# Kernel optimization log

Measured on AMD Instinct MI355X. Metric: run time of the kernel, lower is better.

The kernel has to match this reference:

```python
import jax, jax.numpy as jnp
import numpy as np

B, I, C, K, L = 4, 4, 256, 7, 5
SIZES = [160, 80, 40, 20, 10]


def setup_inputs() -> dict:
    key = jax.random.key(0)
    ks = jax.random.split(key, 10)
    inp = {}
    for i, s in enumerate(SIZES):
        inp[f"feats_x{i}"] = jax.random.normal(ks[i], (B, C, s, s), jnp.float32)
    inp["modulator"] = jax.random.normal(ks[5], (B, I, C, K, K), jnp.float32)
    # conv weights ~ normal_init(std=0.01), biases zero
    inp["pm_w"] = 0.01 * jax.random.normal(ks[6], (L, C, C, K, K), jnp.float32)
    inp["pm_b"] = jnp.zeros((L, C), jnp.float32)
    inp["po_w"] = 0.01 * jax.random.normal(ks[7], (L, C, C), jnp.float32)
    inp["po_b"] = jnp.zeros((L, C), jnp.float32)
    return inp


def reference(feats_x0, feats_x1, feats_x2, feats_x3, feats_x4,
              modulator, pm_w, pm_b, po_w, po_b):
    """Batched version of RPN_Modulator.inference: for every (image i, instance j,
    level k): q = Conv7x7(modulator[i,j]) -> [C,1,1]; out = Conv1x1(q * feats_x[k][i]).
    Vectorized over images and instances instead of nested Python loops."""
    feats = [feats_x0, feats_x1, feats_x2, feats_x3, feats_x4]
    outs = []
    for k in range(L):
        # 7x7 valid conv on a 7x7 crop == full contraction -> per-instance channel vector
        q = jnp.einsum('bichw,ochw->bio', modulator, pm_w[k]) + pm_b[k]  # [B,I,C]
        # channel-wise modulation of the gallery feature map
        m = q[:, :, :, None, None] * feats[k][:, None]                   # [B,I,C,H,W]
        # 1x1 output projection
        o = jnp.einsum('bichw,oc->biohw', m, po_w[k]) \
            + po_b[k][None, None, :, None, None]                          # [B,I,C,H,W]
        outs.append(o)
    return tuple(outs)
```

## Files before the change

### kernel.cpp

```cpp
#include <hip/hip_runtime.h>
#include <hip/hip_bf16.h>


typedef __bf16 bf16x8 __attribute__((ext_vector_type(8)));
typedef float  f32x4  __attribute__((ext_vector_type(4)));
typedef float  f32x16 __attribute__((ext_vector_type(16)));
typedef unsigned short u16;

__device__ __forceinline__ unsigned pack2(float lo, float hi) {
    __hip_bfloat162 h = __float22bfloat162_rn(make_float2(lo, hi));
    union { __hip_bfloat162 h; unsigned u; } cv; cv.h = h; return cv.u;
}

__device__ __forceinline__ void decode_tile(int x, int& k, int& nt, int& N, size_t& oo) {
    if (x < 200)      { k = 0; nt = x;       N = 25600; oo = 0; }
    else if (x < 250) { k = 1; nt = x - 200; N = 6400;  oo = 104857600; }
    else if (x < 263) { k = 2; nt = x - 250; N = 1600;  oo = 131072000; }
    else if (x < 267) { k = 3; nt = x - 263; N = 400;   oo = 137625600; }
    else              { k = 4; nt = x - 267; N = 100;   oo = 139264000; }
}

__global__ __launch_bounds__(256) void k_q(
    const float* __restrict__ modulator,
    const float* __restrict__ pm_w,
    float* __restrict__ qpart)
{
    int o4 = blockIdx.x;
    int k  = blockIdx.y;
    int s  = blockIdx.z;
    int t  = threadIdx.x;
    float acc[4][16];
#pragma unroll
    for (int j = 0; j < 4; ++j)
#pragma unroll
        for (int bi = 0; bi < 16; ++bi) acc[j][bi] = 0.f;
    const float4* mod4 = (const float4*)modulator;
    const float4* wp0 = (const float4*)(pm_w + ((size_t)k * 256 + o4      ) * 12544);
    const float4* wp1 = (const float4*)(pm_w + ((size_t)k * 256 + o4 +  64) * 12544);
    const float4* wp2 = (const float4*)(pm_w + ((size_t)k * 256 + o4 + 128) * 12544);
    const float4* wp3 = (const float4*)(pm_w + ((size_t)k * 256 + o4 + 192) * 12544);
    for (int it = 0; it < 4; ++it) {
        int jj = it * 256 + t;
        if (jj < 784) {
            int jx = s * 784 + jj;
            float4 wv0 = wp0[jx], wv1 = wp1[jx], wv2 = wp2[jx], wv3 = wp3[jx];
#pragma unroll
            for (int bi = 0; bi < 16; ++bi) {
                float4 m = mod4[bi * 3136 + jx];
                acc[0][bi] += wv0.x * m.x + wv0.y * m.y + wv0.z * m.z + wv0.w * m.w;
                acc[1][bi] += wv1.x * m.x + wv1.y * m.y + wv1.z * m.z + wv1.w * m.w;
                acc[2][bi] += wv2.x * m.x + wv2.y * m.y + wv2.z * m.z + wv2.w * m.w;
                acc[3][bi] += wv3.x * m.x + wv3.y * m.y + wv3.z * m.z + wv3.w * m.w;
            }
        }
    }
#pragma unroll
    for (int j = 0; j < 4; ++j)
#pragma unroll
        for (int bi = 0; bi < 16; ++bi)
#pragma unroll
            for (int off = 32; off > 0; off >>= 1)
                acc[j][bi] += __shfl_down(acc[j][bi], off);
    __shared__ float red[4][64];
    int w = t >> 6, lane = t & 63;
    if (lane == 0) {
#pragma unroll
        for (int j = 0; j < 4; ++j)
#pragma unroll
            for (int bi = 0; bi < 16; ++bi) red[w][j * 16 + bi] = acc[j][bi];
    }
    __syncthreads();
    if (t < 64) {
        float v = red[0][t] + red[1][t] + red[2][t] + red[3][t];
        int bi = t & 15;
        int o  = o4 + (t >> 4) * 64;
        qpart[(((size_t)s * 5 + k) * 16 + bi) * 256 + o] = v;
    }
}

__global__ __launch_bounds__(256) void k_w2(
    const float* __restrict__ po_w,
    const float* __restrict__ pm_b,
    const float* __restrict__ qpart,
    u16* __restrict__ w2)
{
    int idx4 = blockIdx.x * 256 + threadIdx.x;
    int c4 = idx4 & 63;
    int o  = (idx4 >> 6) & 255;
    int bi = (idx4 >> 14) & 15;
    int k  = idx4 >> 18;
    size_t qi = ((size_t)(k * 16 + bi)) * 256 + c4 * 4;
    f32x4 q0 = *(const f32x4*)(qpart + qi);
    f32x4 q1 = *(const f32x4*)(qpart + qi + 20480);
    f32x4 q2 = *(const f32x4*)(qpart + qi + 40960);
    f32x4 q3 = *(const f32x4*)(qpart + qi + 61440);
    f32x4 pb = *(const f32x4*)(pm_b + k * 256 + c4 * 4);
    f32x4 q  = q0 + q1 + q2 + q3 + pb;
    f32x4 w  = *(const f32x4*)(po_w + ((size_t)(k * 256 + o)) * 256 + c4 * 4);
    uint2 r;
    r.x = pack2(w[0] * q[0], w[1] * q[1]);
    r.y = pack2(w[2] * q[2], w[3] * q[3]);
    *(uint2*)(w2 + (size_t)idx4 * 4) = r;
}

__global__ __launch_bounds__(512, 4) void k_gemm(
    const float* __restrict__ f0, const float* __restrict__ f1,
    const float* __restrict__ f2, const float* __restrict__ f3,
    const float* __restrict__ f4,
    const u16* __restrict__ w2,
    const float* __restrict__ po_b,
    float* __restrict__ out)
{
    __shared__ __align__(16) u16 ldsB[128 * 256];
    int k, nt, N; size_t oo;
    decode_tile(blockIdx.x, k, nt, N, oo);
    const float* fsrc = (k == 0) ? f0 : (k == 1) ? f1 : (k == 2) ? f2 : (k == 3) ? f3 : f4;
    const int b = blockIdx.y;
    const int t = threadIdx.x;
    const int n0 = nt * 128;

    {
        const int ng = t & 31, grp = t >> 5;
        const bool inb = (n0 + ng * 4) < N;
        const float* s = fsrc + (size_t)b * 256 * N + n0 + ng * 4;
#pragma unroll
        for (int j = 0; j < 4; ++j) {
            int q = j * 16 + grp;
            f32x4 v0 = {0.f,0.f,0.f,0.f}, v1 = {0.f,0.f,0.f,0.f};
            f32x4 v2 = {0.f,0.f,0.f,0.f}, v3 = {0.f,0.f,0.f,0.f};
            if (inb) {
                v0 = *(const f32x4*)(s + (size_t)(4 * q + 0) * N);
                v1 = *(const f32x4*)(s + (size_t)(4 * q + 1) * N);
                v2 = *(const f32x4*)(s + (size_t)(4 * q + 2) * N);
                v3 = *(const f32x4*)(s + (size_t)(4 * q + 3) * N);
            }
#pragma unroll
            for (int e = 0; e < 4; ++e) {
                int n = ng * 4 + e;
                unsigned h = ((unsigned)n & 7u) ^ (((unsigned)n >> 2) & 7u);
                unsigned off = ((unsigned)n << 9) + ((unsigned)q << 3);
                off ^= (h << 4);
                uint2 wv; wv.x = pack2(v0[e], v1[e]); wv.y = pack2(v2[e], v3[e]);
                *(uint2*)((char*)ldsB + off) = wv;
            }
        }
    }
    __syncthreads();

    const int lane = t & 63, w = t >> 6;
    const int l31 = lane & 31, lg5 = lane >> 5;
    const float* pb = po_b + k * 256;
    float* obase0 = out + oo;

    f32x4 bias4[4];
#pragma unroll
    for (int m = 0; m < 4; ++m)
        bias4[m] = *(const f32x4*)(pb + w * 32 + 8 * m + 4 * lg5);

    unsigned mrow[4], mx[4];
#pragma unroll
    for (int ni = 0; ni < 4; ++ni) {
        int row = ni * 32 + l31;
        unsigned h = ((unsigned)row & 7u) ^ (((unsigned)row >> 2) & 7u);
        mrow[ni] = (unsigned)row << 9;
        mx[ni] = ((unsigned)lg5 ^ h) << 4;
    }

#pragma unroll 1
    for (int i = 0; i < 4; ++i) {
        const u16* wsrc = w2 + ((size_t)(k * 16 + b * 4 + i) << 16)
                        + (size_t)(w * 32 + l31) * 256 + lg5 * 8;
        float* obase = obase0 + (size_t)(b * 4 + i) * 256 * N;

        f32x16 acc[4];
#pragma unroll
        for (int ni = 0; ni < 4; ++ni)
#pragma unroll
            for (int q = 0; q < 16; ++q)
                acc[ni][q] = bias4[q >> 2][q & 3];

#pragma unroll 2
        for (int kk = 0; kk < 16; ++kk) {
            bf16x8 a = *(const bf16x8*)(wsrc + kk * 16);
            bf16x8 bb[4];
            unsigned kb = (unsigned)kk << 5;
#pragma unroll
            for (int ni = 0; ni < 4; ++ni)
                bb[ni] = *(const bf16x8*)((const char*)ldsB + (mrow[ni] + (kb ^ mx[ni])));
#pragma unroll
            for (int ni = 0; ni < 4; ++ni)
                acc[ni] = __builtin_amdgcn_mfma_f32_32x32x16_bf16(a, bb[ni], acc[ni], 0, 0, 0);
        }

#pragma unroll
        for (int ni = 0; ni < 4; ++ni) {
            int ocol = n0 + ni * 32 + l31;
            if (ocol < N) {
                float* op = obase + ocol;
#pragma unroll
                for (int q = 0; q < 16; ++q) {
                    int orow = w * 32 + (q & 3) + 8 * (q >> 2) + 4 * lg5;
                    __builtin_nontemporal_store(acc[ni][q], op + (size_t)orow * N);
                }
            }
        }
    }
}

extern "C" void kernel_launch(void* const* d_in, const int* in_sizes, int n_in,
                              void* d_out, int out_size, void* d_ws, size_t ws_size,
                              hipStream_t stream) {
    const float* f0 = (const float*)d_in[0];
    const float* f1 = (const float*)d_in[1];
    const float* f2 = (const float*)d_in[2];
    const float* f3 = (const float*)d_in[3];
    const float* f4 = (const float*)d_in[4];
    const float* modulator = (const float*)d_in[5];
    const float* pm_w = (const float*)d_in[6];
    const float* pm_b = (const float*)d_in[7];
    const float* po_w = (const float*)d_in[8];
    const float* po_b = (const float*)d_in[9];
    float* out = (float*)d_out;

    u16* w2 = (u16*)d_ws;
    float* qpart = (float*)(w2 + (size_t)5 * 16 * 256 * 256);

    k_q<<<dim3(64, 5, 4), 256, 0, stream>>>(modulator, pm_w, qpart);
    k_w2<<<5120, 256, 0, stream>>>(po_w, pm_b, qpart, w2);
    k_gemm<<<dim3(268, 4), 512, 0, stream>>>(f0, f1, f2, f3, f4, w2, po_b, out);
}
```

Baseline: 193.5 us.

## Make GEMM kernel persistent with double-buffered LDS prefetch of next feature tile

Replaces the one-tile-per-block GEMM launch with 512 persistent blocks that loop over 2136 jobs. Each job is a 64-column tile for one batch, half the previous 128 columns. While computing the current tile, the kernel loads the next tile's features into registers and writes them into the alternate LDS buffer, overlapping global loads with MFMA work and output stores. This hides the load latency of each tile's prologue, at the cost of smaller tiles (less reuse of A per LDS load), more registers for staging, and an extra barrier per job.

```diff
diff --git a/kernel.cpp b/kernel.cpp
--- a/kernel.cpp
+++ b/kernel.cpp
@@ -7,17 +7,20 @@
 typedef float  f32x16 __attribute__((ext_vector_type(16)));
 typedef unsigned short u16;
 
+#define NWORK 512
+#define NJOBS 2136
+
 __device__ __forceinline__ unsigned pack2(float lo, float hi) {
     __hip_bfloat162 h = __float22bfloat162_rn(make_float2(lo, hi));
     union { __hip_bfloat162 h; unsigned u; } cv; cv.h = h; return cv.u;
 }
 
 __device__ __forceinline__ void decode_tile(int x, int& k, int& nt, int& N, size_t& oo) {
-    if (x < 200)      { k = 0; nt = x;       N = 25600; oo = 0; }
-    else if (x < 250) { k = 1; nt = x - 200; N = 6400;  oo = 104857600; }
-    else if (x < 263) { k = 2; nt = x - 250; N = 1600;  oo = 131072000; }
-    else if (x < 267) { k = 3; nt = x - 263; N = 400;   oo = 137625600; }
-    else              { k = 4; nt = x - 267; N = 100;   oo = 139264000; }
+    if (x < 400)      { k = 0; nt = x;       N = 25600; oo = 0; }
+    else if (x < 500) { k = 1; nt = x - 400; N = 6400;  oo = 104857600; }
+    else if (x < 525) { k = 2; nt = x - 500; N = 1600;  oo = 131072000; }
+    else if (x < 532) { k = 3; nt = x - 525; N = 400;   oo = 137625600; }
+    else              { k = 4; nt = x - 532; N = 100;   oo = 139264000; }
 }
 
 __global__ __launch_bounds__(256) void k_q(
@@ -103,6 +106,42 @@
     *(uint2*)(w2 + (size_t)idx4 * 4) = r;
 }
 
+
+__device__ __forceinline__ void stage_load(const float* __restrict__ fsrc,
+                                           int b, int N, int n0, int ng, int cq0,
+                                           f32x4 stg[2][4]) {
+    const bool inb = (n0 + ng * 4) < N;
+    const float* s = fsrc + (size_t)b * 256 * N + n0 + ng * 4;
+#pragma unroll
+    for (int jj = 0; jj < 2; ++jj) {
+        int cq = cq0 + 32 * jj;
+#pragma unroll
+        for (int r = 0; r < 4; ++r) {
+            stg[jj][r] = (f32x4){0.f, 0.f, 0.f, 0.f};
+            if (inb) stg[jj][r] = *(const f32x4*)(s + (size_t)(4 * cq + r) * N);
+        }
+    }
+}
+
+__device__ __forceinline__ void stage_write(u16* __restrict__ ldsbuf,
+                                            int ng, int cq0, const f32x4 stg[2][4]) {
+#pragma unroll
+    for (int jj = 0; jj < 2; ++jj) {
+        int cq = cq0 + 32 * jj;
+#pragma unroll
+        for (int e = 0; e < 4; ++e) {
+            int n = ng * 4 + e;
+            unsigned h = ((unsigned)n & 7u) ^ (((unsigned)n >> 2) & 7u);
+            unsigned off = ((unsigned)n << 9) + ((unsigned)cq << 3);
+            off ^= (h << 4);
+            uint2 wv;
+            wv.x = pack2(stg[jj][0][e], stg[jj][1][e]);
+            wv.y = pack2(stg[jj][2][e], stg[jj][3][e]);
+            *(uint2*)((char*)ldsbuf + off) = wv;
+        }
+    }
+}
+
 __global__ __launch_bounds__(512, 4) void k_gemm(
     const float* __restrict__ f0, const float* __restrict__ f1,
     const float* __restrict__ f2, const float* __restrict__ f3,
@@ -111,99 +150,103 @@
     const float* __restrict__ po_b,
     float* __restrict__ out)
 {
-    __shared__ __align__(16) u16 ldsB[128 * 256];
-    int k, nt, N; size_t oo;
-    decode_tile(blockIdx.x, k, nt, N, oo);
-    const float* fsrc = (k == 0) ? f0 : (k == 1) ? f1 : (k == 2) ? f2 : (k == 3) ? f3 : f4;
-    const int b = blockIdx.y;
+    __shared__ __align__(16) u16 lds[2][64 * 256];
     const int t = threadIdx.x;
-    const int n0 = nt * 128;
-
-    {
-        const int ng = t & 31, grp = t >> 5;
-        const bool inb = (n0 + ng * 4) < N;
-        const float* s = fsrc + (size_t)b * 256 * N + n0 + ng * 4;
-#pragma unroll
-        for (int j = 0; j < 4; ++j) {
-            int q = j * 16 + grp;
-            f32x4 v0 = {0.f,0.f,0.f,0.f}, v1 = {0.f,0.f,0.f,0.f};
-            f32x4 v2 = {0.f,0.f,0.f,0.f}, v3 = {0.f,0.f,0.f,0.f};
-            if (inb) {
-                v0 = *(const f32x4*)(s + (size_t)(4 * q + 0) * N);
-                v1 = *(const f32x4*)(s + (size_t)(4 * q + 1) * N);
-                v2 = *(const f32x4*)(s + (size_t)(4 * q + 2) * N);
-                v3 = *(const f32x4*)(s + (size_t)(4 * q + 3) * N);
-            }
-#pragma unroll
-            for (int e = 0; e < 4; ++e) {
-                int n = ng * 4 + e;
-                unsigned h = ((unsigned)n & 7u) ^ (((unsigned)n >> 2) & 7u);
-                unsigned off = ((unsigned)n << 9) + ((unsigned)q << 3);
-                off ^= (h << 4);
-                uint2 wv; wv.x = pack2(v0[e], v1[e]); wv.y = pack2(v2[e], v3[e]);
-                *(uint2*)((char*)ldsB + off) = wv;
-            }
-        }
-    }
-    __syncthreads();
-
     const int lane = t & 63, w = t >> 6;
     const int l31 = lane & 31, lg5 = lane >> 5;
-    const float* pb = po_b + k * 256;
-    float* obase0 = out + oo;
-
-    f32x4 bias4[4];
-#pragma unroll
-    for (int m = 0; m < 4; ++m)
-        bias4[m] = *(const f32x4*)(pb + w * 32 + 8 * m + 4 * lg5);
-
-    unsigned mrow[4], mx[4];
-#pragma unroll
-    for (int ni = 0; ni < 4; ++ni) {
+    const int ng = t & 15, cq0 = t >> 4;
+
+    unsigned mrow[2], mx[2];
+#pragma unroll
+    for (int ni = 0; ni < 2; ++ni) {
         int row = ni * 32 + l31;
         unsigned h = ((unsigned)row & 7u) ^ (((unsigned)row >> 2) & 7u);
         mrow[ni] = (unsigned)row << 9;
         mx[ni] = ((unsigned)lg5 ^ h) << 4;
     }
 
-#pragma unroll 1
-    for (int i = 0; i < 4; ++i) {
-        const u16* wsrc = w2 + ((size_t)(k * 16 + b * 4 + i) << 16)
-                        + (size_t)(w * 32 + l31) * 256 + lg5 * 8;
-        float* obase = obase0 + (size_t)(b * 4 + i) * 256 * N;
-
-        f32x16 acc[4];
-#pragma unroll
-        for (int ni = 0; ni < 4; ++ni)
-#pragma unroll
-            for (int q = 0; q < 16; ++q)
-                acc[ni][q] = bias4[q >> 2][q & 3];
-
-#pragma unroll 2
-        for (int kk = 0; kk < 16; ++kk) {
-            bf16x8 a = *(const bf16x8*)(wsrc + kk * 16);
-            bf16x8 bb[4];
-            unsigned kb = (unsigned)kk << 5;
-#pragma unroll
-            for (int ni = 0; ni < 4; ++ni)
-                bb[ni] = *(const bf16x8*)((const char*)ldsB + (mrow[ni] + (kb ^ mx[ni])));
-#pragma unroll
-            for (int ni = 0; ni < 4; ++ni)
-                acc[ni] = __builtin_amdgcn_mfma_f32_32x32x16_bf16(a, bb[ni], acc[ni], 0, 0, 0);
-        }
-
-#pragma unroll
-        for (int ni = 0; ni < 4; ++ni) {
-            int ocol = n0 + ni * 32 + l31;
-            if (ocol < N) {
-                float* op = obase + ocol;
-#pragma unroll
-                for (int q = 0; q < 16; ++q) {
-                    int orow = w * 32 + (q & 3) + 8 * (q >> 2) + 4 * lg5;
-                    __builtin_nontemporal_store(acc[ni][q], op + (size_t)orow * N);
+    int job = blockIdx.x;
+    int k, nt, N; size_t oo;
+    decode_tile(job >> 2, k, nt, N, oo);
+    int b = job & 3;
+
+    f32x4 stg[2][4];
+    {
+        const float* fsrc = (k == 0) ? f0 : (k == 1) ? f1 : (k == 2) ? f2 : (k == 3) ? f3 : f4;
+        stage_load(fsrc, b, N, nt * 64, ng, cq0, stg);
+        stage_write(lds[0], ng, cq0, stg);
+    }
+    asm volatile("s_waitcnt lgkmcnt(0)" ::: "memory");
+    __builtin_amdgcn_s_barrier();
+
+    int cur = 0;
+    for (;;) {
+        const int n0 = nt * 64;
+        const char* Lc = (const char*)lds[cur];
+        const float* pb = po_b + k * 256;
+        f32x4 bias4[4];
+#pragma unroll
+        for (int m = 0; m < 4; ++m)
+            bias4[m] = *(const f32x4*)(pb + w * 32 + 8 * m + 4 * lg5);
+
+        const int jn = job + NWORK;
+        const bool hn = jn < NJOBS;
+        int k2 = 0, nt2 = 0, N2 = 0, b2 = 0; size_t oo2 = 0;
+        if (hn) { decode_tile(jn >> 2, k2, nt2, N2, oo2); b2 = jn & 3; }
+
+#pragma unroll
+        for (int i = 0; i < 4; ++i) {
+            const u16* wsrc = w2 + ((size_t)(k * 16 + b * 4 + i) << 16)
+                            + (size_t)(w * 32 + l31) * 256 + lg5 * 8;
+            float* obase = out + oo + (size_t)(b * 4 + i) * 256 * N;
+
+            f32x16 acc[2];
+#pragma unroll
+            for (int ni = 0; ni < 2; ++ni)
+#pragma unroll
+                for (int q = 0; q < 16; ++q)
+                    acc[ni][q] = bias4[q >> 2][q & 3];
+
+#pragma unroll 4
+            for (int kk = 0; kk < 16; ++kk) {
+                bf16x8 a = *(const bf16x8*)(wsrc + kk * 16);
+                unsigned kb = (unsigned)kk << 5;
+                bf16x8 bb0 = *(const bf16x8*)(Lc + (mrow[0] + (kb ^ mx[0])));
+                bf16x8 bb1 = *(const bf16x8*)(Lc + (mrow[1] + (kb ^ mx[1])));
+                acc[0] = __builtin_amdgcn_mfma_f32_32x32x16_bf16(a, bb0, acc[0], 0, 0, 0);
+                acc[1] = __builtin_amdgcn_mfma_f32_32x32x16_bf16(a, bb1, acc[1], 0, 0, 0);
+            }
+
+#pragma unroll
+            for (int ni = 0; ni < 2; ++ni) {
+                int ocol = n0 + ni * 32 + l31;
+                if (ocol < N) {
+                    float* op = obase + ocol;
+#pragma unroll
+                    for (int q = 0; q < 16; ++q) {
+                        int orow = w * 32 + (q & 3) + 8 * (q >> 2) + 4 * lg5;
+                        __builtin_nontemporal_store(acc[ni][q], op + (size_t)orow * N);
+                    }
                 }
             }
-        }
+
+            if (i == 0 && hn) {
+                __builtin_amdgcn_sched_barrier(0);
+                const float* fs2 = (k2 == 0) ? f0 : (k2 == 1) ? f1 : (k2 == 2) ? f2
+                                 : (k2 == 3) ? f3 : f4;
+                stage_load(fs2, b2, N2, nt2 * 64, ng, cq0, stg);
+                __builtin_amdgcn_sched_barrier(0);
+            }
+            if (i == 2 && hn) {
+                stage_write((u16*)lds[cur ^ 1], ng, cq0, stg);
+            }
+        }
+
+        asm volatile("s_waitcnt lgkmcnt(0)" ::: "memory");
+        __builtin_amdgcn_s_barrier();
+
+        if (!hn) break;
+        job = jn; k = k2; nt = nt2; N = N2; oo = oo2; b = b2; cur ^= 1;
     }
 }
 
@@ -227,5 +270,5 @@
 
     k_q<<<dim3(64, 5, 4), 256, 0, stream>>>(modulator, pm_w, qpart);
     k_w2<<<5120, 256, 0, stream>>>(po_w, pm_b, qpart, w2);
-    k_gemm<<<dim3(268, 4), 512, 0, stream>>>(f0, f1, f2, f3, f4, w2, po_b, out);
-}
+    k_gemm<<<NWORK, 512, 0, stream>>>(f0, f1, f2, f3, f4, w2, po_b, out);
+}
```

Result: slower. 255.2 us (+31.9%).

## Remap k_q threads over (instance, k-slice) and use plain output stores

Applied to the files above, without the earlier changes.

Restructures the modulator projection kernel so each lane handles one image-instance and a strided slice of the 7x7xC contraction. Each thread now keeps 4 accumulators instead of 64, which removes the large register footprint and the 64-value wavefront shuffle reductions in exchange for less reuse of weights across instances. The GEMM epilogue also switches from nontemporal stores to ordinary global stores, which changes the cache behaviour of the large output write.

```diff
diff --git a/kernel.cpp b/kernel.cpp
--- a/kernel.cpp
+++ b/kernel.cpp
@@ -25,56 +25,48 @@
     const float* __restrict__ pm_w,
     float* __restrict__ qpart)
 {
-    int o4 = blockIdx.x;
-    int k  = blockIdx.y;
-    int s  = blockIdx.z;
-    int t  = threadIdx.x;
-    float acc[4][16];
-#pragma unroll
-    for (int j = 0; j < 4; ++j)
-#pragma unroll
-        for (int bi = 0; bi < 16; ++bi) acc[j][bi] = 0.f;
-    const float4* mod4 = (const float4*)modulator;
-    const float4* wp0 = (const float4*)(pm_w + ((size_t)k * 256 + o4      ) * 12544);
-    const float4* wp1 = (const float4*)(pm_w + ((size_t)k * 256 + o4 +  64) * 12544);
-    const float4* wp2 = (const float4*)(pm_w + ((size_t)k * 256 + o4 + 128) * 12544);
-    const float4* wp3 = (const float4*)(pm_w + ((size_t)k * 256 + o4 + 192) * 12544);
-    for (int it = 0; it < 4; ++it) {
-        int jj = it * 256 + t;
-        if (jj < 784) {
-            int jx = s * 784 + jj;
-            float4 wv0 = wp0[jx], wv1 = wp1[jx], wv2 = wp2[jx], wv3 = wp3[jx];
-#pragma unroll
-            for (int bi = 0; bi < 16; ++bi) {
-                float4 m = mod4[bi * 3136 + jx];
-                acc[0][bi] += wv0.x * m.x + wv0.y * m.y + wv0.z * m.z + wv0.w * m.w;
-                acc[1][bi] += wv1.x * m.x + wv1.y * m.y + wv1.z * m.z + wv1.w * m.w;
-                acc[2][bi] += wv2.x * m.x + wv2.y * m.y + wv2.z * m.z + wv2.w * m.w;
-                acc[3][bi] += wv3.x * m.x + wv3.y * m.y + wv3.z * m.z + wv3.w * m.w;
-            }
-        }
-    }
-#pragma unroll
-    for (int j = 0; j < 4; ++j)
-#pragma unroll
-        for (int bi = 0; bi < 16; ++bi)
-#pragma unroll
-            for (int off = 32; off > 0; off >>= 1)
-                acc[j][bi] += __shfl_down(acc[j][bi], off);
+    const int o4 = blockIdx.x;
+    const int k  = blockIdx.y;
+    const int s  = blockIdx.z;
+    const int t  = threadIdx.x;
+    const int w  = t >> 6, lane = t & 63;
+    const int bi = lane >> 2, sub = lane & 3;
+    const int sg = w * 4 + sub;
+
+    const float4* mod4 = (const float4*)modulator + (size_t)bi * 3136 + s * 784 + sg;
+    const float4* wp0 = (const float4*)(pm_w + ((size_t)k * 256 + o4      ) * 12544) + s * 784 + sg;
+    const float4* wp1 = (const float4*)(pm_w + ((size_t)k * 256 + o4 +  64) * 12544) + s * 784 + sg;
+    const float4* wp2 = (const float4*)(pm_w + ((size_t)k * 256 + o4 + 128) * 12544) + s * 784 + sg;
+    const float4* wp3 = (const float4*)(pm_w + ((size_t)k * 256 + o4 + 192) * 12544) + s * 784 + sg;
+
+    float a0 = 0.f, a1 = 0.f, a2 = 0.f, a3 = 0.f;
+#pragma unroll 7
+    for (int i = 0; i < 49; ++i) {
+        float4 m = mod4[i * 16];
+        float4 x0 = wp0[i * 16], x1 = wp1[i * 16], x2 = wp2[i * 16], x3 = wp3[i * 16];
+        a0 += x0.x * m.x + x0.y * m.y + x0.z * m.z + x0.w * m.w;
+        a1 += x1.x * m.x + x1.y * m.y + x1.z * m.z + x1.w * m.w;
+        a2 += x2.x * m.x + x2.y * m.y + x2.z * m.z + x2.w * m.w;
+        a3 += x3.x * m.x + x3.y * m.y + x3.z * m.z + x3.w * m.w;
+    }
+    a0 += __shfl_down(a0, 1); a1 += __shfl_down(a1, 1);
+    a2 += __shfl_down(a2, 1); a3 += __shfl_down(a3, 1);
+    a0 += __shfl_down(a0, 2); a1 += __shfl_down(a1, 2);
+    a2 += __shfl_down(a2, 2); a3 += __shfl_down(a3, 2);
+
     __shared__ float red[4][64];
-    int w = t >> 6, lane = t & 63;
-    if (lane == 0) {
-#pragma unroll
-        for (int j = 0; j < 4; ++j)
-#pragma unroll
-            for (int bi = 0; bi < 16; ++bi) red[w][j * 16 + bi] = acc[j][bi];
+    if (sub == 0) {
+        red[w][bi * 4 + 0] = a0;
+        red[w][bi * 4 + 1] = a1;
+        red[w][bi * 4 + 2] = a2;
+        red[w][bi * 4 + 3] = a3;
     }
     __syncthreads();
     if (t < 64) {
         float v = red[0][t] + red[1][t] + red[2][t] + red[3][t];
-        int bi = t & 15;
-        int o  = o4 + (t >> 4) * 64;
-        qpart[(((size_t)s * 5 + k) * 16 + bi) * 256 + o] = v;
+        int bii = t >> 2;
+        int o   = o4 + (t & 3) * 64;
+        qpart[(((size_t)s * 5 + k) * 16 + bii) * 256 + o] = v;
     }
 }
 
@@ -200,7 +192,7 @@
 #pragma unroll
                 for (int q = 0; q < 16; ++q) {
                     int orow = w * 32 + (q & 3) + 8 * (q >> 2) + 4 * lg5;
-                    __builtin_nontemporal_store(acc[ni][q], op + (size_t)orow * N);
+                    op[(size_t)orow * N] = acc[ni][q];
                 }
             }
         }
```

After: 293.8 us. 51.9% more time.
